# Optimization experiments

Hardware: AMD Instinct MI355X
Metric: run time of the kernel (lower is better)

Reference implementation:

```python
import jax, jax.numpy as jnp
import numpy as np

N, M = 60000, 12       # atoms, neighbors per atom
D = 64                 # atom_fea_len
NBR = 41               # nbr_fea_len
B, NA = 1200, 50       # crystals x atoms per crystal; B*NA == N
EPS = 1e-5


def setup_inputs() -> dict:
    key = jax.random.key(0)
    ks = jax.random.split(key, 8)
    def rn(k, shape, scale=0.05):
        return jax.random.normal(k, shape, jnp.float32) * scale
    return {
        "atom_in_fea": jax.random.normal(ks[0], (N, D), jnp.float32),
        "nbr_fea": jax.random.normal(ks[1], (N, M, NBR), jnp.float32),
        "adj": jax.random.uniform(ks[2], (B, NA, NA), jnp.float32),
        "w1": rn(ks[3], (D, D)), "b1": jnp.zeros((D,), jnp.float32),
        "w2": rn(ks[4], (D, D)), "b2": jnp.zeros((D,), jnp.float32),
        "tln1_g": jnp.ones((D,), jnp.float32), "tln1_b": jnp.zeros((D,), jnp.float32),
        "tln2_g": jnp.ones((D,), jnp.float32), "tln2_b": jnp.zeros((D,), jnp.float32),
        "fc_w": rn(ks[5], (2 * D + NBR, 2 * D)), "fc_b": jnp.zeros((2 * D,), jnp.float32),
        "bn1_g": jnp.ones((2 * D,), jnp.float32), "bn1_b": jnp.zeros((2 * D,), jnp.float32),
        "bn2_g": jnp.ones((D,), jnp.float32), "bn2_b": jnp.zeros((D,), jnp.float32),
        "nbr_fea_idx": jax.random.randint(ks[6], (N, M), 0, N, jnp.int32),
        "crystal_atom_idx": jnp.arange(N, dtype=jnp.int32).reshape(B, NA),
    }


def _layernorm(x, g, b):
    mu = x.mean(-1, keepdims=True)
    var = x.var(-1, keepdims=True)  # biased, matches torch LayerNorm
    return (x - mu) * jax.lax.rsqrt(var + EPS) * g + b


def _batchnorm(x, g, b):
    # training-mode BatchNorm1d over all leading dims (biased var, matches torch)
    x2 = x.reshape(-1, x.shape[-1])
    mu = x2.mean(0)
    var = x2.var(0)
    return (x - mu) * jax.lax.rsqrt(var + EPS) * g + b


def _forward(atom_in_fea, nbr_fea, adj, w1, b1, w2, b2, tln1_g, tln1_b,
             tln2_g, tln2_b, fc_w, fc_b, bn1_g, bn1_b, bn2_g, bn2_b,
             nbr_fea_idx, crystal_atom_idx):
    # gather neighbor features from ORIGINAL atom features (as in torch code)
    atom_nbr_fea = atom_in_fea[nbr_fea_idx]              # [N, M, D]

    # graph transformer (1 layer, no q/k/v projections), equal-size crystals
    src = atom_in_fea[crystal_atom_idx]                  # [B, NA, D]
    scale = 1.0 / jnp.sqrt(jnp.float32(D))
    scores = jnp.einsum('bnd,bmd->bnm', src, src) * scale * adj
    attn = jax.nn.softmax(scores, axis=-1)
    src2 = jnp.einsum('bnm,bmd->bnd', attn, src)
    src = _layernorm(src + src2, tln1_g, tln1_b)         # dropout = identity (eval)
    h = jax.nn.relu(src @ w1 + b1) @ w2 + b2
    src = _layernorm(src + h, tln2_g, tln2_b)
    atom_tf = src.reshape(N, D)                          # [N, D]

    # concat [self_transformed | neighbor_orig | bond], linear, BN, gate, reduce
    total = jnp.concatenate([
        jnp.broadcast_to(atom_tf[:, None, :], (N, M, D)),
        atom_nbr_fea,
        nbr_fea,
    ], axis=2)                                           # [N, M, 2D+NBR]
    gated = total @ fc_w + fc_b                          # [N, M, 2D]
    gated = _batchnorm(gated, bn1_g, bn1_b)
    nbr_filter = jax.nn.sigmoid(gated[..., :D])
    nbr_core = jax.nn.softplus(gated[..., D:])
    nbr_sumed = jnp.sum(nbr_filter * nbr_core, axis=1)   # [N, D]
    nbr_sumed = _batchnorm(nbr_sumed, bn2_g, bn2_b)
    return jax.nn.softplus(atom_tf + nbr_sumed)          # [N, D]


def reference(atom_in_fea, nbr_fea, adj, w1, b1, w2, b2, tln1_g, tln1_b,
              tln2_g, tln2_b, fc_w, fc_b, bn1_g, bn1_b, bn2_g, bn2_b,
              nbr_fea_idx, crystal_atom_idx):
    return _forward(atom_in_fea, nbr_fea, adj, w1, b1, w2, b2, tln1_g, tln1_b,
                    tln2_g, tln2_b, fc_w, fc_b, bn1_g, bn1_b, bn2_g, bn2_b,
                    nbr_fea_idx, crystal_atom_idx)
```

## Files before the change

### kernel.cpp

```cpp
#include <hip/hip_runtime.h>
#include <math.h>

#define N_ATOMS 60000
#define M_NBR   12
#define D_FEA   64
#define NBR_FEA 41
#define B_CRY   1200
#define NA_CRY  50
#define EPSV    1e-5f

#define NBLK_MAIN 2048

__device__ __forceinline__ float wsum(float v){
#pragma unroll
  for (int o = 32; o > 0; o >>= 1) v += __shfl_xor(v, o, 64);
  return v;
}
__device__ __forceinline__ float wmax64(float v){
#pragma unroll
  for (int o = 32; o > 0; o >>= 1) v = fmaxf(v, __shfl_xor(v, o, 64));
  return v;
}
__device__ __forceinline__ float softplusf(float x){
  return fmaxf(x, 0.f) + __logf(1.f + __expf(-fabsf(x)));
}
__device__ __forceinline__ float sigmoidf(float x){
  return 1.f / (1.f + __expf(-x));
}
__device__ __forceinline__ unsigned bf16_rne(float x){
  unsigned u = __float_as_uint(x);
  return (u + 0x7fffu + ((u >> 16) & 1u)) >> 16;
}
__device__ __forceinline__ unsigned pack2(float lo, float hi){
  return bf16_rne(lo) | (bf16_rne(hi) << 16);
}
__device__ __forceinline__ float unlo(unsigned u){ return __uint_as_float(u << 16); }
__device__ __forceinline__ float unhi(unsigned u){ return __uint_as_float(u & 0xffff0000u); }

__global__ __launch_bounds__(512, 4) void k_transformer(
    const float* __restrict__ atom_in, const float* __restrict__ adj,
    const float* __restrict__ w1, const float* __restrict__ b1,
    const float* __restrict__ w2, const float* __restrict__ b2,
    const float* __restrict__ g1v, const float* __restrict__ be1,
    const float* __restrict__ g2v, const float* __restrict__ be2,
    const int* __restrict__ cidx, const float* __restrict__ fc_w,
    const float* __restrict__ fc_b, float* __restrict__ atom_tf,
    unsigned* __restrict__ proj1p, unsigned* __restrict__ proj2p)
{
  __shared__ float s_a[NA_CRY * D_FEA];
  __shared__ float s_b[D_FEA * (NA_CRY + 1)];
  __shared__ float s_c[NA_CRY * D_FEA];
  __shared__ int   s_gi[NA_CRY];

  const int tid  = threadIdx.x;
  const int b    = blockIdx.x;
  const int lane = tid & 63;
  const int w    = tid >> 6;

  if (tid < NA_CRY) s_gi[tid] = cidx[b * NA_CRY + tid];
  for (int p = tid; p < NA_CRY * D_FEA; p += 512){
    int i = p >> 6, d = p & 63;
    int a = cidx[b * NA_CRY + i];
    float v = atom_in[a * D_FEA + d];
    s_a[p] = v;
    s_b[d * (NA_CRY + 1) + i] = v;
  }
  __syncthreads();

  const float scale = 0.125f;
  {
    const float* adjb = adj + (size_t)b * NA_CRY * NA_CRY;
    for (int t = tid; t < 625; t += 512){
      int i0 = (t / 25) * 2, j0 = (t % 25) * 2;
      float a00 = 0.f, a01 = 0.f, a10 = 0.f, a11 = 0.f;
#pragma unroll 8
      for (int d = 0; d < D_FEA; ++d){
        float va0 = s_a[i0 * D_FEA + d];
        float va1 = s_a[(i0 + 1) * D_FEA + d];
        float vb0 = s_b[d * (NA_CRY + 1) + j0];
        float vb1 = s_b[d * (NA_CRY + 1) + j0 + 1];
        a00 += va0 * vb0; a01 += va0 * vb1;
        a10 += va1 * vb0; a11 += va1 * vb1;
      }
      s_c[i0 * NA_CRY + j0]           = a00 * scale * adjb[i0 * NA_CRY + j0];
      s_c[i0 * NA_CRY + j0 + 1]       = a01 * scale * adjb[i0 * NA_CRY + j0 + 1];
      s_c[(i0 + 1) * NA_CRY + j0]     = a10 * scale * adjb[(i0 + 1) * NA_CRY + j0];
      s_c[(i0 + 1) * NA_CRY + j0 + 1] = a11 * scale * adjb[(i0 + 1) * NA_CRY + j0 + 1];
    }
  }
  __syncthreads();

  for (int r = w; r < NA_CRY; r += 8){
    float v = (lane < NA_CRY) ? s_c[r * NA_CRY + lane] : -1e30f;
    float mx = wmax64(v);
    float e = (lane < NA_CRY) ? __expf(v - mx) : 0.f;
    float s = wsum(e);
    if (lane < NA_CRY) s_c[r * NA_CRY + lane] = e / s;
  }
  __syncthreads();

  for (int t = tid; t < 25 * D_FEA; t += 512){
    int nh = t >> 6, d = t & 63;
    int n0 = nh * 2, n1 = n0 + 1;
    float x0 = 0.f, x1 = 0.f;
#pragma unroll 10
    for (int m = 0; m < NA_CRY; ++m){
      float sa = s_a[m * D_FEA + d];
      x0 += s_c[n0 * NA_CRY + m] * sa;
      x1 += s_c[n1 * NA_CRY + m] * sa;
    }
    s_b[n0 * D_FEA + d] = s_a[n0 * D_FEA + d] + x0;
    s_b[n1 * D_FEA + d] = s_a[n1 * D_FEA + d] + x1;
  }
  __syncthreads();

  for (int r = w; r < NA_CRY; r += 8){
    float x = s_b[r * D_FEA + lane];
    float mu = wsum(x) * (1.f / 64.f);
    float dx = x - mu;
    float var = wsum(dx * dx) * (1.f / 64.f);
    s_a[r * D_FEA + lane] = dx * rsqrtf(var + EPSV) * g1v[lane] + be1[lane];
  }
  __syncthreads();

  for (int n0 = w * 2; n0 < NA_CRY; n0 += 16){
    const int n1 = n0 + 1;
    float x00 = 0.f, x01 = 0.f, x10 = 0.f, x11 = 0.f;
#pragma unroll
    for (int k = 0; k < D_FEA; k += 2){
      float wv0 = w1[k * D_FEA + lane];
      float wv1 = w1[(k + 1) * D_FEA + lane];
      x00 += s_a[n0 * D_FEA + k] * wv0;
      x01 += s_a[n0 * D_FEA + k + 1] * wv1;
      x10 += s_a[n1 * D_FEA + k] * wv0;
      x11 += s_a[n1 * D_FEA + k + 1] * wv1;
    }
    float bb = b1[lane];
    s_c[n0 * D_FEA + lane] = fmaxf(bb + x00 + x01, 0.f);
    s_c[n1 * D_FEA + lane] = fmaxf(bb + x10 + x11, 0.f);
  }
  __syncthreads();

  for (int n0 = w * 2; n0 < NA_CRY; n0 += 16){
    const int n1 = n0 + 1;
    float x00 = 0.f, x01 = 0.f, x10 = 0.f, x11 = 0.f;
#pragma unroll
    for (int k = 0; k < D_FEA; k += 2){
      float wv0 = w2[k * D_FEA + lane];
      float wv1 = w2[(k + 1) * D_FEA + lane];
      x00 += s_c[n0 * D_FEA + k] * wv0;
      x01 += s_c[n0 * D_FEA + k + 1] * wv1;
      x10 += s_c[n1 * D_FEA + k] * wv0;
      x11 += s_c[n1 * D_FEA + k + 1] * wv1;
    }
    float bb = b2[lane];
    float t0 = s_a[n0 * D_FEA + lane] + bb + x00 + x01;
    float t1 = s_a[n1 * D_FEA + lane] + bb + x10 + x11;
    {
      float mu = wsum(t0) * (1.f / 64.f);
      float dx = t0 - mu;
      float var = wsum(dx * dx) * (1.f / 64.f);
      float res = dx * rsqrtf(var + EPSV) * g2v[lane] + be2[lane];
      atom_tf[(size_t)(b * NA_CRY + n0) * D_FEA + lane] = res;
      s_a[n0 * D_FEA + lane] = res;
    }
    {
      float mu = wsum(t1) * (1.f / 64.f);
      float dx = t1 - mu;
      float var = wsum(dx * dx) * (1.f / 64.f);
      float res = dx * rsqrtf(var + EPSV) * g2v[lane] + be2[lane];
      atom_tf[(size_t)(b * NA_CRY + n1) * D_FEA + lane] = res;
      s_a[n1 * D_FEA + lane] = res;
    }
  }
  __syncthreads();

  for (int p = tid; p < NA_CRY * D_FEA; p += 512){
    int i = p >> 6, d = p & 63;
    s_c[p] = atom_in[(size_t)s_gi[i] * D_FEA + d];
  }
  __syncthreads();

  for (int n0 = w * 4; n0 < NA_CRY; n0 += 32){
    const int nb = (n0 + 1 < NA_CRY) ? n0 + 1 : NA_CRY - 1;
    const int nc = (n0 + 2 < NA_CRY) ? n0 + 2 : NA_CRY - 1;
    const int nd = (n0 + 3 < NA_CRY) ? n0 + 3 : NA_CRY - 1;
    const int c = lane;
    const float bb0 = fc_b[c], bb1 = fc_b[64 + c];
    float A1 = bb0, A2 = bb1, A3 = 0.f, A4 = 0.f;
    float B1 = bb0, B2 = bb1, B3 = 0.f, B4 = 0.f;
    float C1 = bb0, C2 = bb1, C3 = 0.f, C4 = 0.f;
    float D1 = bb0, D2 = bb1, D3 = 0.f, D4 = 0.f;
#pragma unroll 4
    for (int k = 0; k < D_FEA; ++k){
      float w0 = fc_w[k * 128 + c];
      float w6 = fc_w[k * 128 + 64 + c];
      float v0 = fc_w[(64 + k) * 128 + c];
      float v6 = fc_w[(64 + k) * 128 + 64 + c];
      float ta = s_a[n0 * 64 + k], tb = s_a[nb * 64 + k];
      float tc = s_a[nc * 64 + k], td = s_a[nd * 64 + k];
      float sa = s_c[n0 * 64 + k], sb = s_c[nb * 64 + k];
      float sc = s_c[nc * 64 + k], sd = s_c[nd * 64 + k];
      A1 += ta * w0; A2 += ta * w6; A3 += sa * v0; A4 += sa * v6;
      B1 += tb * w0; B2 += tb * w6; B3 += sb * v0; B4 += sb * v6;
      C1 += tc * w0; C2 += tc * w6; C3 += sc * v0; C4 += sc * v6;
      D1 += td * w0; D2 += td * w6; D3 += sd * v0; D4 += sd * v6;
    }
    proj1p[(size_t)(b * NA_CRY + n0) * 64 + c] = pack2(A1, A2);
    proj2p[(size_t)s_gi[n0] * 64 + c] = pack2(A3, A4);
    if (n0 + 1 < NA_CRY){
      proj1p[(size_t)(b * NA_CRY + nb) * 64 + c] = pack2(B1, B2);
      proj2p[(size_t)s_gi[nb] * 64 + c] = pack2(B3, B4);
    }
    if (n0 + 2 < NA_CRY){
      proj1p[(size_t)(b * NA_CRY + nc) * 64 + c] = pack2(C1, C2);
      proj2p[(size_t)s_gi[nc] * 64 + c] = pack2(C3, C4);
    }
    if (n0 + 3 < NA_CRY){
      proj1p[(size_t)(b * NA_CRY + nd) * 64 + c] = pack2(D1, D2);
      proj2p[(size_t)s_gi[nd] * 64 + c] = pack2(D3, D4);
    }
  }
}

#define LOADRW(MM) unsigned rw##MM = proj2p[(size_t)__builtin_amdgcn_readfirstlane(jrow[MM]) * 64 + lane];

#define STAGE(AA, BUF) { \
    const float* srcp = nbr_fea + (size_t)(AA) * (M_NBR * NBR_FEA); \
    float* dstp = s_frow + (w * 2 + (BUF)) * 512; \
    __builtin_amdgcn_global_load_lds(srcp + lane * 4, dstp, 16, 0, 0); \
    if (lane < 59) \
      __builtin_amdgcn_global_load_lds(srcp + 256 + lane * 4, dstp + 256, 16, 0, 0); \
  }

#define GBODY(MM) { \
    float g0 = p10 + unlo(rw##MM); \
    float g1 = p11 + unhi(rw##MM); \
    _Pragma("unroll") \
    for (int k = 0; k < NBR_FEA; ++k){ \
      float aa = fr[MM * NBR_FEA + k]; \
      g0 += aa * unlo(wbp[k]); \
      g1 += aa * unhi(wbp[k]); \
    } \
    if (STORE) gated[(size_t)(base + MM) * 64 + lane] = pack2(g0, g1); \
    s0 += g0; q0 += g0 * g0; \
    s1 += g1; q1 += g1 * g1; }

template<int STORE>
__global__ __launch_bounds__(256) void k_stats(
    const float* __restrict__ nbr_fea, const int* __restrict__ nbr_idx,
    const float* __restrict__ fc_w, const unsigned* __restrict__ proj1p,
    const unsigned* __restrict__ proj2p, float* __restrict__ part1,
    unsigned* __restrict__ gated)
{
  __shared__ float red[1024];
  __shared__ float s_frow[4 * 2 * 512];
  const int tid = threadIdx.x, lane = tid & 63, w = tid >> 6;

  unsigned wbp[NBR_FEA];
#pragma unroll
  for (int k = 0; k < NBR_FEA; ++k){
    float w0 = fc_w[(128 + k) * 128 + lane];
    float w1 = fc_w[(128 + k) * 128 + 64 + lane];
    wbp[k] = pack2(w0, w1);
  }

  const int gw = blockIdx.x * 4 + w, nw = gridDim.x * 4;
  const int q = N_ATOMS / nw, rr = N_ATOMS % nw;
  const int a0 = gw * q + (gw < rr ? gw : rr);
  const int a1 = a0 + q + (gw < rr ? 1 : 0);
  float s0 = 0.f, s1 = 0.f, q0 = 0.f, q1 = 0.f;
  int cur = 0;
  if (a0 < a1){ STAGE(a0, 0); }
  for (int a = a0; a < a1; ++a){
    const int au = __builtin_amdgcn_readfirstlane(a);
    const int base = au * M_NBR;
    const int* jrow = nbr_idx + base;
    unsigned p1v = proj1p[(size_t)au * 64 + lane];
    LOADRW(0) LOADRW(1) LOADRW(2) LOADRW(3) LOADRW(4) LOADRW(5)
    LOADRW(6) LOADRW(7) LOADRW(8) LOADRW(9) LOADRW(10) LOADRW(11)
    const int anext = (a + 1 < a1) ? (a + 1) : a;
    STAGE(anext, cur ^ 1);
    asm volatile("s_waitcnt vmcnt(2)" ::: "memory");
    const float* fr = s_frow + (w * 2 + cur) * 512;
    const float p10 = unlo(p1v), p11 = unhi(p1v);
    GBODY(0) GBODY(1) GBODY(2) GBODY(3) GBODY(4) GBODY(5)
    GBODY(6) GBODY(7) GBODY(8) GBODY(9) GBODY(10) GBODY(11)
    cur ^= 1;
  }
  red[w * 256 + lane]        = s0;
  red[w * 256 + 64 + lane]   = s1;
  red[w * 256 + 128 + lane]  = q0;
  red[w * 256 + 192 + lane]  = q1;
  __syncthreads();
  float v = red[tid] + red[256 + tid] + red[512 + tid] + red[768 + tid];
  part1[blockIdx.x * 256 + tid] = v;
}

__global__ __launch_bounds__(256) void k_stats_fin(
    const float* __restrict__ part1, const float* __restrict__ bn1_g,
    const float* __restrict__ bn1_b, float* __restrict__ stats1)
{
  __shared__ float red[256];
  const int c = blockIdx.x;
  const int t = threadIdx.x;
  float s = 0.f, q = 0.f;
#pragma unroll
  for (int i = t; i < NBLK_MAIN; i += 256){
    s += part1[(size_t)i * 256 + c];
    q += part1[(size_t)i * 256 + 128 + c];
  }
  red[t] = s; __syncthreads();
  for (int o = 128; o > 0; o >>= 1){ if (t < o) red[t] += red[t + o]; __syncthreads(); }
  float sumv = red[0]; __syncthreads();
  red[t] = q; __syncthreads();
  for (int o = 128; o > 0; o >>= 1){ if (t < o) red[t] += red[t + o]; __syncthreads(); }
  if (t == 0){
    const float inv = 1.f / (float)(N_ATOMS * M_NBR);
    float mu = sumv * inv;
    float var = red[0] * inv - mu * mu;
    float sc = bn1_g[c] * rsqrtf(var + EPSV);
    stats1[c] = sc;
    stats1[128 + c] = bn1_b[c] - mu * sc;
  }
}

__global__ __launch_bounds__(256) void k_reduce_g(
    const unsigned* __restrict__ gated, const float* __restrict__ stats1,
    float* __restrict__ nbr_sumed, float* __restrict__ part2)
{
  __shared__ float red[512];
  const int tid = threadIdx.x, lane = tid & 63, w = tid >> 6;
  const float sc0 = stats1[lane],       sc1 = stats1[64 + lane];
  const float tc0 = stats1[128 + lane], tc1 = stats1[192 + lane];
  const int wg = blockIdx.x * 4 + w, nw = gridDim.x * 4;
  float bs = 0.f, bq = 0.f;
  for (int a = wg; a < N_ATOMS; a += nw){
    const size_t base = (size_t)a * M_NBR * 64 + lane;
    float acc = 0.f;
#pragma unroll
    for (int m = 0; m < M_NBR; ++m){
      unsigned gv = gated[base + m * 64];
      acc += sigmoidf(unlo(gv) * sc0 + tc0) * softplusf(unhi(gv) * sc1 + tc1);
    }
    nbr_sumed[(size_t)a * 64 + lane] = acc;
    bs += acc; bq += acc * acc;
  }
  red[w * 128 + lane]      = bs;
  red[w * 128 + 64 + lane] = bq;
  __syncthreads();
  if (tid < 128){
    float v = red[tid] + red[128 + tid] + red[256 + tid] + red[384 + tid];
    part2[blockIdx.x * 128 + tid] = v;
  }
}

#define GBODYR(MM) { \
    const float* frow = nbr_fea + (size_t)(base + MM) * NBR_FEA; \
    float g0 = p10 + unlo(rw##MM); \
    float g1 = p11 + unhi(rw##MM); \
    _Pragma("unroll") \
    for (int k = 0; k < NBR_FEA; ++k){ \
      float aa = frow[k]; \
      g0 += aa * unlo(wbp[k]); \
      g1 += aa * unhi(wbp[k]); \
    } \
    acc += sigmoidf(g0 * sc0 + tc0) * softplusf(g1 * sc1 + tc1); }

__global__ __launch_bounds__(256) void k_reduce_r(
    const float* __restrict__ nbr_fea, const int* __restrict__ nbr_idx,
    const float* __restrict__ fc_w, const unsigned* __restrict__ proj1p,
    const unsigned* __restrict__ proj2p, const float* __restrict__ stats1,
    float* __restrict__ nbr_sumed, float* __restrict__ part2)
{
  __shared__ float red[512];
  const int tid = threadIdx.x, lane = tid & 63, w = tid >> 6;
  unsigned wbp[NBR_FEA];
#pragma unroll
  for (int k = 0; k < NBR_FEA; ++k){
    float w0 = fc_w[(128 + k) * 128 + lane];
    float w1 = fc_w[(128 + k) * 128 + 64 + lane];
    wbp[k] = pack2(w0, w1);
  }
  const float sc0 = stats1[lane],       sc1 = stats1[64 + lane];
  const float tc0 = stats1[128 + lane], tc1 = stats1[192 + lane];
  const int gw = blockIdx.x * 4 + w, nw = gridDim.x * 4;
  const int q = N_ATOMS / nw, rr = N_ATOMS % nw;
  const int a0 = gw * q + (gw < rr ? gw : rr);
  const int a1 = a0 + q + (gw < rr ? 1 : 0);
  float bs = 0.f, bq = 0.f;
  for (int a = a0; a < a1; ++a){
    const int au = __builtin_amdgcn_readfirstlane(a);
    const int base = au * M_NBR;
    const int* jrow = nbr_idx + base;
    unsigned p1v = proj1p[(size_t)au * 64 + lane];
    LOADRW(0) LOADRW(1) LOADRW(2) LOADRW(3) LOADRW(4) LOADRW(5)
    LOADRW(6) LOADRW(7) LOADRW(8) LOADRW(9) LOADRW(10) LOADRW(11)
    const float p10 = unlo(p1v), p11 = unhi(p1v);
    float acc = 0.f;
    GBODYR(0) GBODYR(1) GBODYR(2) GBODYR(3) GBODYR(4) GBODYR(5)
    GBODYR(6) GBODYR(7) GBODYR(8) GBODYR(9) GBODYR(10) GBODYR(11)
    nbr_sumed[(size_t)au * 64 + lane] = acc;
    bs += acc; bq += acc * acc;
  }
  red[w * 128 + lane]      = bs;
  red[w * 128 + 64 + lane] = bq;
  __syncthreads();
  if (tid < 128){
    float v = red[tid] + red[128 + tid] + red[256 + tid] + red[384 + tid];
    part2[blockIdx.x * 128 + tid] = v;
  }
}

__global__ __launch_bounds__(256) void k_red_fin(
    const float* __restrict__ part2, const float* __restrict__ bn2_g,
    const float* __restrict__ bn2_b, float* __restrict__ stats2)
{
  __shared__ float red[256];
  const int c = blockIdx.x;
  const int t = threadIdx.x;
  float s = 0.f, q = 0.f;
#pragma unroll
  for (int i = t; i < NBLK_MAIN; i += 256){
    s += part2[(size_t)i * 128 + c];
    q += part2[(size_t)i * 128 + 64 + c];
  }
  red[t] = s; __syncthreads();
  for (int o = 128; o > 0; o >>= 1){ if (t < o) red[t] += red[t + o]; __syncthreads(); }
  float sumv = red[0]; __syncthreads();
  red[t] = q; __syncthreads();
  for (int o = 128; o > 0; o >>= 1){ if (t < o) red[t] += red[t + o]; __syncthreads(); }
  if (t == 0){
    const float inv = 1.f / (float)N_ATOMS;
    float mu = sumv * inv;
    float var = red[0] * inv - mu * mu;
    float sc = bn2_g[c] * rsqrtf(var + EPSV);
    stats2[c] = sc;
    stats2[64 + c] = bn2_b[c] - mu * sc;
  }
}

__global__ __launch_bounds__(256) void k_final(
    const float* __restrict__ atom_tf, const float* __restrict__ ns,
    const float* __restrict__ stats2, float* __restrict__ out)
{
  int i = blockIdx.x * 256 + threadIdx.x;
  if (i >= N_ATOMS * 64) return;
  int c = i & 63;
  float x = atom_tf[i] + ns[i] * stats2[c] + stats2[64 + c];
  out[i] = softplusf(x);
}

extern "C" void kernel_launch(void* const* d_in, const int* in_sizes, int n_in,
                              void* d_out, int out_size, void* d_ws, size_t ws_size,
                              hipStream_t stream)
{
  const float* atom_in = (const float*)d_in[0];
  const float* nbr_fea = (const float*)d_in[1];
  const float* adj     = (const float*)d_in[2];
  const float* w1 = (const float*)d_in[3];
  const float* b1 = (const float*)d_in[4];
  const float* w2 = (const float*)d_in[5];
  const float* b2 = (const float*)d_in[6];
  const float* tln1_g = (const float*)d_in[7];
  const float* tln1_b = (const float*)d_in[8];
  const float* tln2_g = (const float*)d_in[9];
  const float* tln2_b = (const float*)d_in[10];
  const float* fc_w = (const float*)d_in[11];
  const float* fc_b = (const float*)d_in[12];
  const float* bn1_g = (const float*)d_in[13];
  const float* bn1_b = (const float*)d_in[14];
  const float* bn2_g = (const float*)d_in[15];
  const float* bn2_b = (const float*)d_in[16];
  const int* nbr_idx = (const int*)d_in[17];
  const int* cidx    = (const int*)d_in[18];
  float* out = (float*)d_out;

  char* ws = (char*)d_ws;
  size_t off = 0;
  float* atom_tf = (float*)(ws + off);    off += (size_t)N_ATOMS * 64 * 4;
  unsigned* proj1p = (unsigned*)(ws + off); off += (size_t)N_ATOMS * 64 * 4;
  unsigned* proj2p = (unsigned*)(ws + off); off += (size_t)N_ATOMS * 64 * 4;
  float* nbr_sumed = (float*)(ws + off);  off += (size_t)N_ATOMS * 64 * 4;
  float* part1 = (float*)(ws + off);      off += (size_t)NBLK_MAIN * 256 * 4;
  float* stats1 = (float*)(ws + off);     off += 256 * 4;
  float* part2 = (float*)(ws + off);      off += (size_t)NBLK_MAIN * 128 * 4;
  float* stats2 = (float*)(ws + off);     off += 128 * 4;
  unsigned* gated = (unsigned*)(ws + off);
  const size_t need_gated = off + (size_t)N_ATOMS * M_NBR * 64 * 4;
  const bool use_gated = (ws_size >= need_gated);

  k_transformer<<<B_CRY, 512, 0, stream>>>(atom_in, adj, w1, b1, w2, b2,
      tln1_g, tln1_b, tln2_g, tln2_b, cidx, fc_w, fc_b, atom_tf, proj1p, proj2p);
  if (use_gated){
    k_stats<1><<<NBLK_MAIN, 256, 0, stream>>>(nbr_fea, nbr_idx, fc_w, proj1p,
        proj2p, part1, gated);
    k_stats_fin<<<128, 256, 0, stream>>>(part1, bn1_g, bn1_b, stats1);
    k_reduce_g<<<NBLK_MAIN, 256, 0, stream>>>(gated, stats1, nbr_sumed, part2);
  } else {
    k_stats<0><<<NBLK_MAIN, 256, 0, stream>>>(nbr_fea, nbr_idx, fc_w, proj1p,
        proj2p, part1, gated);
    k_stats_fin<<<128, 256, 0, stream>>>(part1, bn1_g, bn1_b, stats1);
    k_reduce_r<<<NBLK_MAIN, 256, 0, stream>>>(nbr_fea, nbr_idx, fc_w, proj1p,
        proj2p, stats1, nbr_sumed, part2);
  }
  k_red_fin<<<64, 256, 0, stream>>>(part2, bn2_g, bn2_b, stats2);
  k_final<<<(N_ATOMS * 64 + 255) / 256, 256, 0, stream>>>(atom_tf, nbr_sumed, stats2, out);
}
```

Measured before the change: 347.3 us.

## Split transformer kernel into attention and wave-parallel feed-forward kernels

```diff
diff --git a/kernel.cpp b/kernel.cpp
--- a/kernel.cpp
+++ b/kernel.cpp
@@ -37,31 +37,24 @@
 __device__ __forceinline__ float unlo(unsigned u){ return __uint_as_float(u << 16); }
 __device__ __forceinline__ float unhi(unsigned u){ return __uint_as_float(u & 0xffff0000u); }
 
-__global__ __launch_bounds__(512, 4) void k_transformer(
+__global__ __launch_bounds__(512, 4) void k_attn(
     const float* __restrict__ atom_in, const float* __restrict__ adj,
-    const float* __restrict__ w1, const float* __restrict__ b1,
-    const float* __restrict__ w2, const float* __restrict__ b2,
     const float* __restrict__ g1v, const float* __restrict__ be1,
-    const float* __restrict__ g2v, const float* __restrict__ be2,
-    const int* __restrict__ cidx, const float* __restrict__ fc_w,
-    const float* __restrict__ fc_b, float* __restrict__ atom_tf,
-    unsigned* __restrict__ proj1p, unsigned* __restrict__ proj2p)
+    const int* __restrict__ cidx, float* __restrict__ ln1)
 {
   __shared__ float s_a[NA_CRY * D_FEA];
   __shared__ float s_b[D_FEA * (NA_CRY + 1)];
   __shared__ float s_c[NA_CRY * D_FEA];
-  __shared__ int   s_gi[NA_CRY];
 
   const int tid  = threadIdx.x;
   const int b    = blockIdx.x;
   const int lane = tid & 63;
   const int w    = tid >> 6;
 
-  if (tid < NA_CRY) s_gi[tid] = cidx[b * NA_CRY + tid];
   for (int p = tid; p < NA_CRY * D_FEA; p += 512){
     int i = p >> 6, d = p & 63;
     int a = cidx[b * NA_CRY + i];
-    float v = atom_in[a * D_FEA + d];
+    float v = atom_in[(size_t)a * D_FEA + d];
     s_a[p] = v;
     s_b[d * (NA_CRY + 1) + i] = v;
   }
@@ -119,107 +112,117 @@
     float mu = wsum(x) * (1.f / 64.f);
     float dx = x - mu;
     float var = wsum(dx * dx) * (1.f / 64.f);
-    s_a[r * D_FEA + lane] = dx * rsqrtf(var + EPSV) * g1v[lane] + be1[lane];
-  }
-  __syncthreads();
-
-  for (int n0 = w * 2; n0 < NA_CRY; n0 += 16){
-    const int n1 = n0 + 1;
-    float x00 = 0.f, x01 = 0.f, x10 = 0.f, x11 = 0.f;
-#pragma unroll
+    ln1[(size_t)(b * NA_CRY + r) * D_FEA + lane] =
+        dx * rsqrtf(var + EPSV) * g1v[lane] + be1[lane];
+  }
+}
+
+__global__ __launch_bounds__(256) void k_ff(
+    const float* __restrict__ ln1, const float* __restrict__ atom_in,
+    const int* __restrict__ cidx,
+    const float* __restrict__ w1, const float* __restrict__ b1,
+    const float* __restrict__ w2, const float* __restrict__ b2,
+    const float* __restrict__ g2v, const float* __restrict__ be2,
+    const float* __restrict__ fc_w, const float* __restrict__ fc_b,
+    float* __restrict__ atom_tf, unsigned* __restrict__ proj1p,
+    unsigned* __restrict__ proj2p)
+{
+  __shared__ float sl[4][8][64];
+  const int tid = threadIdx.x, lane = tid & 63, w = tid >> 6;
+  float (*A)[64] = &sl[w][0];
+  float (*Bs)[64] = &sl[w][4];
+
+  const int gw = blockIdx.x * 4 + w, nw = gridDim.x * 4;
+  const int NGRP = N_ATOMS / 4;
+  for (int g = gw; g < NGRP; g += nw){
+    const int r0 = g * 4;
+    float ln0 = ln1[(size_t)(r0 + 0) * 64 + lane];
+    float ln1v = ln1[(size_t)(r0 + 1) * 64 + lane];
+    float ln2 = ln1[(size_t)(r0 + 2) * 64 + lane];
+    float ln3 = ln1[(size_t)(r0 + 3) * 64 + lane];
+    A[0][lane] = ln0; A[1][lane] = ln1v; A[2][lane] = ln2; A[3][lane] = ln3;
+    __builtin_amdgcn_s_waitcnt(0);
+
+    float h0a = 0.f, h1a = 0.f, h2a = 0.f, h3a = 0.f;
+    float h0b = 0.f, h1b = 0.f, h2b = 0.f, h3b = 0.f;
+#pragma unroll 8
     for (int k = 0; k < D_FEA; k += 2){
       float wv0 = w1[k * D_FEA + lane];
       float wv1 = w1[(k + 1) * D_FEA + lane];
-      x00 += s_a[n0 * D_FEA + k] * wv0;
-      x01 += s_a[n0 * D_FEA + k + 1] * wv1;
-      x10 += s_a[n1 * D_FEA + k] * wv0;
-      x11 += s_a[n1 * D_FEA + k + 1] * wv1;
+      h0a += A[0][k] * wv0; h0b += A[0][k + 1] * wv1;
+      h1a += A[1][k] * wv0; h1b += A[1][k + 1] * wv1;
+      h2a += A[2][k] * wv0; h2b += A[2][k + 1] * wv1;
+      h3a += A[3][k] * wv0; h3b += A[3][k + 1] * wv1;
     }
-    float bb = b1[lane];
-    s_c[n0 * D_FEA + lane] = fmaxf(bb + x00 + x01, 0.f);
-    s_c[n1 * D_FEA + lane] = fmaxf(bb + x10 + x11, 0.f);
-  }
-  __syncthreads();
-
-  for (int n0 = w * 2; n0 < NA_CRY; n0 += 16){
-    const int n1 = n0 + 1;
-    float x00 = 0.f, x01 = 0.f, x10 = 0.f, x11 = 0.f;
-#pragma unroll
+    float bb1 = b1[lane];
+    float h0 = fmaxf(bb1 + h0a + h0b, 0.f);
+    float h1 = fmaxf(bb1 + h1a + h1b, 0.f);
+    float h2 = fmaxf(bb1 + h2a + h2b, 0.f);
+    float h3 = fmaxf(bb1 + h3a + h3b, 0.f);
+    Bs[0][lane] = h0; Bs[1][lane] = h1; Bs[2][lane] = h2; Bs[3][lane] = h3;
+    __builtin_amdgcn_s_waitcnt(0);
+
+    float t0a = 0.f, t1a = 0.f, t2a = 0.f, t3a = 0.f;
+    float t0b = 0.f, t1b = 0.f, t2b = 0.f, t3b = 0.f;
+#pragma unroll 8
     for (int k = 0; k < D_FEA; k += 2){
       float wv0 = w2[k * D_FEA + lane];
       float wv1 = w2[(k + 1) * D_FEA + lane];
-      x00 += s_c[n0 * D_FEA + k] * wv0;
-      x01 += s_c[n0 * D_FEA + k + 1] * wv1;
-      x10 += s_c[n1 * D_FEA + k] * wv0;
-      x11 += s_c[n1 * D_FEA + k + 1] * wv1;
+      t0a += Bs[0][k] * wv0; t0b += Bs[0][k + 1] * wv1;
+      t1a += Bs[1][k] * wv0; t1b += Bs[1][k + 1] * wv1;
+      t2a += Bs[2][k] * wv0; t2b += Bs[2][k + 1] * wv1;
+      t3a += Bs[3][k] * wv0; t3b += Bs[3][k + 1] * wv1;
     }
-    float bb = b2[lane];
-    float t0 = s_a[n0 * D_FEA + lane] + bb + x00 + x01;
-    float t1 = s_a[n1 * D_FEA + lane] + bb + x10 + x11;
-    {
-      float mu = wsum(t0) * (1.f / 64.f);
-      float dx = t0 - mu;
-      float var = wsum(dx * dx) * (1.f / 64.f);
-      float res = dx * rsqrtf(var + EPSV) * g2v[lane] + be2[lane];
-      atom_tf[(size_t)(b * NA_CRY + n0) * D_FEA + lane] = res;
-      s_a[n0 * D_FEA + lane] = res;
-    }
-    {
-      float mu = wsum(t1) * (1.f / 64.f);
-      float dx = t1 - mu;
-      float var = wsum(dx * dx) * (1.f / 64.f);
-      float res = dx * rsqrtf(var + EPSV) * g2v[lane] + be2[lane];
-      atom_tf[(size_t)(b * NA_CRY + n1) * D_FEA + lane] = res;
-      s_a[n1 * D_FEA + lane] = res;
-    }
-  }
-  __syncthreads();
-
-  for (int p = tid; p < NA_CRY * D_FEA; p += 512){
-    int i = p >> 6, d = p & 63;
-    s_c[p] = atom_in[(size_t)s_gi[i] * D_FEA + d];
-  }
-  __syncthreads();
-
-  for (int n0 = w * 4; n0 < NA_CRY; n0 += 32){
-    const int nb = (n0 + 1 < NA_CRY) ? n0 + 1 : NA_CRY - 1;
-    const int nc = (n0 + 2 < NA_CRY) ? n0 + 2 : NA_CRY - 1;
-    const int nd = (n0 + 3 < NA_CRY) ? n0 + 3 : NA_CRY - 1;
-    const int c = lane;
-    const float bb0 = fc_b[c], bb1 = fc_b[64 + c];
-    float A1 = bb0, A2 = bb1, A3 = 0.f, A4 = 0.f;
-    float B1 = bb0, B2 = bb1, B3 = 0.f, B4 = 0.f;
-    float C1 = bb0, C2 = bb1, C3 = 0.f, C4 = 0.f;
-    float D1 = bb0, D2 = bb1, D3 = 0.f, D4 = 0.f;
+    float bb2 = b2[lane];
+    float t0 = ln0 + bb2 + t0a + t0b;
+    float t1 = ln1v + bb2 + t1a + t1b;
+    float t2 = ln2 + bb2 + t2a + t2b;
+    float t3 = ln3 + bb2 + t3a + t3b;
+
+    float gv = g2v[lane], bv = be2[lane];
+#define LN2ROW(TT, JJ) { \
+      float mu = wsum(TT) * (1.f / 64.f); \
+      float dx = (TT) - mu; \
+      float var = wsum(dx * dx) * (1.f / 64.f); \
+      float res = dx * rsqrtf(var + EPSV) * gv + bv; \
+      atom_tf[(size_t)(r0 + JJ) * 64 + lane] = res; \
+      A[JJ][lane] = res; }
+    LN2ROW(t0, 0) LN2ROW(t1, 1) LN2ROW(t2, 2) LN2ROW(t3, 3)
+#undef LN2ROW
+
+    const int ga0 = cidx[r0], ga1 = cidx[r0 + 1], ga2 = cidx[r0 + 2], ga3 = cidx[r0 + 3];
+    Bs[0][lane] = atom_in[(size_t)ga0 * 64 + lane];
+    Bs[1][lane] = atom_in[(size_t)ga1 * 64 + lane];
+    Bs[2][lane] = atom_in[(size_t)ga2 * 64 + lane];
+    Bs[3][lane] = atom_in[(size_t)ga3 * 64 + lane];
+    __builtin_amdgcn_s_waitcnt(0);
+
+    const float bb0 = fc_b[lane], bb6 = fc_b[64 + lane];
+    float A1 = bb0, A2 = bb6, A3 = 0.f, A4 = 0.f;
+    float B1 = bb0, B2 = bb6, B3 = 0.f, B4 = 0.f;
+    float C1 = bb0, C2 = bb6, C3 = 0.f, C4 = 0.f;
+    float D1 = bb0, D2 = bb6, D3 = 0.f, D4 = 0.f;
 #pragma unroll 4
     for (int k = 0; k < D_FEA; ++k){
-      float w0 = fc_w[k * 128 + c];
-      float w6 = fc_w[k * 128 + 64 + c];
-      float v0 = fc_w[(64 + k) * 128 + c];
-      float v6 = fc_w[(64 + k) * 128 + 64 + c];
-      float ta = s_a[n0 * 64 + k], tb = s_a[nb * 64 + k];
-      float tc = s_a[nc * 64 + k], td = s_a[nd * 64 + k];
-      float sa = s_c[n0 * 64 + k], sb = s_c[nb * 64 + k];
-      float sc = s_c[nc * 64 + k], sd = s_c[nd * 64 + k];
+      float w0 = fc_w[k * 128 + lane];
+      float w6 = fc_w[k * 128 + 64 + lane];
+      float v0 = fc_w[(64 + k) * 128 + lane];
+      float v6 = fc_w[(64 + k) * 128 + 64 + lane];
+      float ta = A[0][k], tb = A[1][k], tc = A[2][k], td = A[3][k];
+      float sa = Bs[0][k], sb = Bs[1][k], sc = Bs[2][k], sd = Bs[3][k];
       A1 += ta * w0; A2 += ta * w6; A3 += sa * v0; A4 += sa * v6;
       B1 += tb * w0; B2 += tb * w6; B3 += sb * v0; B4 += sb * v6;
       C1 += tc * w0; C2 += tc * w6; C3 += sc * v0; C4 += sc * v6;
       D1 += td * w0; D2 += td * w6; D3 += sd * v0; D4 += sd * v6;
     }
-    proj1p[(size_t)(b * NA_CRY + n0) * 64 + c] = pack2(A1, A2);
-    proj2p[(size_t)s_gi[n0] * 64 + c] = pack2(A3, A4);
-    if (n0 + 1 < NA_CRY){
-      proj1p[(size_t)(b * NA_CRY + nb) * 64 + c] = pack2(B1, B2);
-      proj2p[(size_t)s_gi[nb] * 64 + c] = pack2(B3, B4);
-    }
-    if (n0 + 2 < NA_CRY){
-      proj1p[(size_t)(b * NA_CRY + nc) * 64 + c] = pack2(C1, C2);
-      proj2p[(size_t)s_gi[nc] * 64 + c] = pack2(C3, C4);
-    }
-    if (n0 + 3 < NA_CRY){
-      proj1p[(size_t)(b * NA_CRY + nd) * 64 + c] = pack2(D1, D2);
-      proj2p[(size_t)s_gi[nd] * 64 + c] = pack2(D3, D4);
-    }
+    proj1p[(size_t)(r0 + 0) * 64 + lane] = pack2(A1, A2);
+    proj1p[(size_t)(r0 + 1) * 64 + lane] = pack2(B1, B2);
+    proj1p[(size_t)(r0 + 2) * 64 + lane] = pack2(C1, C2);
+    proj1p[(size_t)(r0 + 3) * 64 + lane] = pack2(D1, D2);
+    proj2p[(size_t)ga0 * 64 + lane] = pack2(A3, A4);
+    proj2p[(size_t)ga1 * 64 + lane] = pack2(B3, B4);
+    proj2p[(size_t)ga2 * 64 + lane] = pack2(C3, C4);
+    proj2p[(size_t)ga3 * 64 + lane] = pack2(D3, D4);
   }
 }
 
@@ -490,8 +493,11 @@
   const size_t need_gated = off + (size_t)N_ATOMS * M_NBR * 64 * 4;
   const bool use_gated = (ws_size >= need_gated);
 
-  k_transformer<<<B_CRY, 512, 0, stream>>>(atom_in, adj, w1, b1, w2, b2,
-      tln1_g, tln1_b, tln2_g, tln2_b, cidx, fc_w, fc_b, atom_tf, proj1p, proj2p);
+  float* ln1 = nbr_sumed;
+
+  k_attn<<<B_CRY, 512, 0, stream>>>(atom_in, adj, tln1_g, tln1_b, cidx, ln1);
+  k_ff<<<2048, 256, 0, stream>>>(ln1, atom_in, cidx, w1, b1, w2, b2,
+      tln2_g, tln2_b, fc_w, fc_b, atom_tf, proj1p, proj2p);
   if (use_gated){
     k_stats<1><<<NBLK_MAIN, 256, 0, stream>>>(nbr_fea, nbr_idx, fc_w, proj1p,
         proj2p, part1, gated);
```

After: 341.3 us. Within noise of the previous version (-1.7%).
